# Kernel tuning notes

Hardware: AMD Instinct MI355X
Metric: run time of the kernel (lower is better)

## Reference

```python
import jax, jax.numpy as jnp
import numpy as np

KS = 3      # kernel_size
PAD = 1     # padding
DIL = 2     # dilation


def conv2d(x, w, b=None, stride=1, padding=0):
    out = jax.lax.conv_general_dilated(
        x, w, (stride, stride), [(padding, padding)] * 2,
        dimension_numbers=("NCHW", "OIHW", "NCHW"))
    if b is not None:
        out = out + b[None, :, None, None]
    return out


def setup_inputs() -> dict:
    key = jax.random.key(0)
    ks = jax.random.split(key, 6)
    b, inc, outc, H, W = 2, 256, 256, 96, 96
    x = jax.random.normal(ks[0], (b, inc, H, W), jnp.float32)
    w_p = jax.random.normal(ks[1], (2 * KS * KS, inc, 3, 3), jnp.float32) * 0.01
    b_p = jax.random.normal(ks[2], (2 * KS * KS,), jnp.float32) * 0.01
    w_ad = jax.random.normal(ks[3], (KS, inc, 3, 3), jnp.float32) * 0.01
    b_ad = jax.random.normal(ks[4], (KS,), jnp.float32) * 0.01
    w_conv = jax.random.normal(ks[5], (outc, inc, KS, KS), jnp.float32) * 0.02
    return {"x": x, "w_p": w_p, "b_p": b_p, "w_ad": w_ad, "b_ad": b_ad, "w_conv": w_conv}


def reference(x, w_p, b_p, w_ad, b_ad, w_conv):
    b, c, H, W = x.shape
    N = KS * KS

    offset = conv2d(x, w_p, b_p, stride=1, padding=1)                    # [b,2N,H,W]
    ad_base = 1.0 - jax.nn.sigmoid(conv2d(x, w_ad, b_ad, stride=1, padding=1))  # [b,KS,H,W]
    ad = jnp.tile(ad_base, (1, 2 * KS, 1, 1)) * DIL                      # [b,2N,H,W]

    # p_n: per-kernel-tap offsets (x-part first, then y-part), meshgrid 'ij'
    r = jnp.arange(-(KS - 1) // 2, (KS - 1) // 2 + 1, dtype=jnp.float32)
    pnx, pny = jnp.meshgrid(r, r, indexing="ij")
    p_n = jnp.concatenate([pnx.ravel(), pny.ravel()])[None, :, None, None]  # [1,2N,1,1]

    # p_0: base sampling grid in padded-image coords (starts at 1)
    p0x = jnp.broadcast_to(jnp.arange(1, H + 1, dtype=jnp.float32)[:, None], (H, W))
    p0y = jnp.broadcast_to(jnp.arange(1, W + 1, dtype=jnp.float32)[None, :], (H, W))
    p_0 = jnp.concatenate([jnp.tile(p0x[None, None], (1, N, 1, 1)),
                           jnp.tile(p0y[None, None], (1, N, 1, 1))], axis=1)  # [1,2N,H,W]

    p = p_0 + p_n + offset + ad * p_n                                    # [b,2N,H,W]
    p = jnp.transpose(p, (0, 2, 3, 1))                                   # [b,H,W,2N]

    xp = jnp.pad(x, ((0, 0), (0, 0), (PAD, PAD), (PAD, PAD)))
    Hp, Wp = xp.shape[2], xp.shape[3]

    q_lt = jnp.floor(jax.lax.stop_gradient(p))
    q_rb = q_lt + 1

    def clampxy(q):
        return jnp.concatenate([jnp.clip(q[..., :N], 0, Hp - 1),
                                jnp.clip(q[..., N:], 0, Wp - 1)], -1).astype(jnp.int32)

    q_lt = clampxy(q_lt)
    q_rb = clampxy(q_rb)
    q_lb = jnp.concatenate([q_lt[..., :N], q_rb[..., N:]], -1)
    q_rt = jnp.concatenate([q_rb[..., :N], q_lt[..., N:]], -1)

    mask = jnp.concatenate(
        [(p[..., :N] < PAD) | (p[..., :N] > Hp - 1 - PAD),
         (p[..., N:] < PAD) | (p[..., N:] > Wp - 1 - PAD)], -1)
    mask = jax.lax.stop_gradient(mask).astype(p.dtype)
    floor_p = p - (p - jnp.floor(p))  # == floor(p) but with zero gradient, as in torch
    p = p * (1 - mask) + floor_p * mask
    p = jnp.concatenate([jnp.clip(p[..., :N], 0, Hp - 1),
                         jnp.clip(p[..., N:], 0, Wp - 1)], -1)

    px, py = p[..., :N], p[..., N:]
    f = lambda q: q.astype(p.dtype)
    g_lt = (1 + (f(q_lt[..., :N]) - px)) * (1 + (f(q_lt[..., N:]) - py))
    g_rb = (1 - (f(q_rb[..., :N]) - px)) * (1 - (f(q_rb[..., N:]) - py))
    g_lb = (1 + (f(q_lb[..., :N]) - px)) * (1 - (f(q_lb[..., N:]) - py))
    g_rt = (1 - (f(q_rt[..., :N]) - px)) * (1 + (f(q_rt[..., N:]) - py))

    xf = xp.reshape(b, c, Hp * Wp)

    def gather(xb, q):  # xb [c,L], q [H,W,2N] -> [c,H,W,N]
        idx = q[..., :N] * Wp + q[..., N:]
        return xb[:, idx]

    gq = jax.vmap(gather)
    x_lt = gq(xf, q_lt)
    x_rb = gq(xf, q_rb)
    x_lb = gq(xf, q_lb)
    x_rt = gq(xf, q_rt)

    x_off = (g_lt[:, None] * x_lt + g_rb[:, None] * x_rb +
             g_lb[:, None] * x_lb + g_rt[:, None] * x_rt)  # [b,c,H,W,N]

    # N index k = kx*KS + ky -> place at (i*KS+kx, j*KS+ky)
    x_off = x_off.reshape(b, c, H, W, KS, KS)
    x_off = jnp.transpose(x_off, (0, 1, 2, 4, 3, 5)).reshape(b, c, H * KS, W * KS)

    return conv2d(x_off, w_conv, None, stride=KS, padding=0)  # [b,outc,H,W]
```

## Files before the change

kernel.cpp:

```cpp
#include <hip/hip_runtime.h>
#include <math.h>

typedef unsigned short u16;
typedef unsigned int   u32;

typedef __attribute__((ext_vector_type(8))) _Float16 f16x8;
typedef __attribute__((ext_vector_type(4))) float    f32x4;

#define NB   2
#define C    256
#define H    96
#define W    96
#define HW   (H*W)
#define HP   98
#define OC   256
#define KDIM (9*C)
#define NS   (NB*HW)

#define PARTIAL_OFF  0
#define XP_OFF       13934592
#define AHI_OFF      33603584
#define ALO_OFF      34783232
#define IDX_OFF      35962880
#define G_OFF        38617088

__device__ __forceinline__ u16 h2u(_Float16 h) {
  return __builtin_bit_cast(unsigned short, h);
}
__device__ __forceinline__ void split16(float v, u16& hi, u16& lo) {
  _Float16 h = (_Float16)v;
  float r = v - (float)h;
  _Float16 l = (_Float16)r;
  hi = h2u(h); lo = h2u(l);
}
__device__ __forceinline__ void sync_lds() {
  asm volatile("s_waitcnt lgkmcnt(0)\n\ts_barrier" ::: "memory");
}

__global__ __launch_bounds__(256) void prep1(
    const float* __restrict__ x, const float* __restrict__ w_p,
    const float* __restrict__ w_ad, const float* __restrict__ w_conv,
    float* __restrict__ partial, float* __restrict__ xp,
    u16* __restrict__ A_hi, u16* __restrict__ A_lo) {
  __shared__ float smem[4224];
  int bx = blockIdx.x;
  int tid = threadIdx.x;

  if (bx < 288) {
    int cg = bx & 1; int chunk = (bx >> 1) & 7; int r = bx >> 4;
    int tile = r % 9; int n = r / 9;
    int h0 = (tile / 3) * 32, w0 = (tile % 3) * 32;
    int chB = cg * 11; int chN = cg ? 10 : 11;

    for (int idx = tid; idx < 3168; idx += 256) {
      int tap = idx % 9; int r2 = idx / 9; int chl = r2 % 11; int cc = r2 / 11;
      int ch = chB + chl; int gc = chunk*32 + cc;
      if (ch < 21) {
        float v = (ch < 18) ? w_p[((size_t)ch*C + gc)*9 + tap]
                            : w_ad[((size_t)(ch-18)*C + gc)*9 + tap];
        smem[(cc*11 + chl)*12 + tap] = v;
      }
    }
    __syncthreads();

    int row = tid >> 3, col0 = (tid & 7) * 4;
    int h = h0 + row, w = w0 + col0;

    float acc[11][4];
    #pragma unroll
    for (int i = 0; i < 11; i++)
      { acc[i][0]=0.f; acc[i][1]=0.f; acc[i][2]=0.f; acc[i][3]=0.f; }

    const float* xn = x + (size_t)(n*C + chunk*32) * HW;
    for (int cc = 0; cc < 32; cc++) {
      const float* xc = xn + cc * HW;
      float xr[3][6];
      #pragma unroll
      for (int di = 0; di < 3; di++) {
        int hg = h + di - 1;
        bool hok = ((unsigned)hg < 96u);
        #pragma unroll
        for (int jj = 0; jj < 6; jj++) {
          int wg = w + jj - 1;
          bool ok = hok && ((unsigned)wg < 96u);
          xr[di][jj] = ok ? xc[hg*W + wg] : 0.f;
        }
      }
      #pragma unroll
      for (int chl = 0; chl < 11; chl++) {
        if (chl < chN) {
          const float* wv = &smem[(cc*11 + chl)*12];
          float4 wa = *(const float4*)(wv);
          float4 wb = *(const float4*)(wv + 4);
          float  w8 = wv[8];
          float wt[9] = {wa.x, wa.y, wa.z, wa.w, wb.x, wb.y, wb.z, wb.w, w8};
          #pragma unroll
          for (int di = 0; di < 3; di++)
            #pragma unroll
            for (int dj = 0; dj < 3; dj++) {
              float wgt = wt[di*3 + dj];
              #pragma unroll
              for (int j = 0; j < 4; j++)
                acc[chl][j] = fmaf(xr[di][dj + j], wgt, acc[chl][j]);
            }
        }
      }
    }
    #pragma unroll
    for (int chl = 0; chl < 11; chl++) {
      if (chl < chN) {
        int off = ((chunk*2 + n)*21 + chB + chl)*HW + h*W + w;
        *(float4*)(partial + off) = make_float4(acc[chl][0], acc[chl][1],
                                                acc[chl][2], acc[chl][3]);
      }
    }

  } else if (bx < 1440) {
    int pb = bx - 288;
    int n = pb / 576; int r = pb % 576;
    int cb = r / 144; int hwb = r % 144;
    int c0 = cb * 64, hw0 = hwb * 64;
    int ii = tid & 63; int cl4 = tid >> 6;
    #pragma unroll
    for (int r2 = 0; r2 < 16; r2++) {
      int c_l = cl4*16 + r2;
      smem[c_l*65 + ii] = x[(size_t)(n*C + c0 + c_l)*HW + hw0 + ii];
    }
    __syncthreads();
    int hw = hw0 + ii;
    int h = hw / W, w = hw % W;
    float* dst = xp + ((size_t)(n*HP + h + 1)*HP + (w + 1))*C + c0 + cl4*16;
    #pragma unroll
    for (int q = 0; q < 4; q++) {
      *(float4*)(dst + q*4) = make_float4(smem[(cl4*16 + q*4 + 0)*65 + ii],
                                          smem[(cl4*16 + q*4 + 1)*65 + ii],
                                          smem[(cl4*16 + q*4 + 2)*65 + ii],
                                          smem[(cl4*16 + q*4 + 3)*65 + ii]);
    }

  } else {
    int pb = bx - 1440;
    int t = pb*256 + tid;
    int e0 = t*8;
    int lane = (e0 >> 3) & 63;
    int mi   = (e0 >> 9) & 3;
    int mw   = (e0 >> 11) & 1;
    int rr   = e0 >> 12; int itg = rr % 72; int mo = rr / 72;
    int o = mo*128 + mw*64 + mi*16 + (lane & 15);
    int kcb = itg*32 + (lane >> 4)*8;
    #pragma unroll
    for (int j2 = 0; j2 < 8; j2++) {
      int kc = kcb + j2; int k = kc >> 8; int c = kc & 255;
      float a = w_conv[((size_t)o*C + c)*9 + k];
      u16 hi, lo; split16(a, hi, lo);
      A_hi[e0 + j2] = hi; A_lo[e0 + j2] = lo;
    }
  }
}

__global__ __launch_bounds__(256) void taps2(
    const float* __restrict__ partial, const float* __restrict__ b_p,
    const float* __restrict__ b_ad,
    int* __restrict__ idx_arr, float* __restrict__ g_arr) {
  int e = blockIdx.x * 256 + threadIdx.x;
  int k = e / NS; int s = e % NS;
  int n = s / HW; int hw = s % HW;
  int h = hw / W, w = hw % W;
  int ka = 18 + (k % 3);
  float offx = 0.f, offy = 0.f, za = 0.f;
  #pragma unroll
  for (int chunk = 0; chunk < 8; chunk++) {
    const float* pb2 = partial + (size_t)((chunk*2 + n)*21)*HW + hw;
    offx += pb2[(size_t)k*HW];
    offy += pb2[(size_t)(k+9)*HW];
    za   += pb2[(size_t)ka*HW];
  }
  offx += b_p[k]; offy += b_p[k+9];
  za   += b_ad[k % 3];
  float a2 = 2.0f / (1.0f + expf(za));

  float ri = (float)(k / 3) - 1.0f, rj = (float)(k % 3) - 1.0f;
  float px = (float)(h + 1) + ri + offx + a2 * ri;
  float py = (float)(w + 1) + rj + offy + a2 * rj;
  float fx = floorf(px), fy = floorf(py);
  int qltx = min(max((int)fx, 0), 97);
  int qlty = min(max((int)fy, 0), 97);
  int qrbx = min(max((int)fx + 1, 0), 97);
  int qrby = min(max((int)fy + 1, 0), 97);
  bool mx = (px < 1.0f) || (px > 96.0f);
  bool my = (py < 1.0f) || (py > 96.0f);
  float pxm = mx ? fx : px;
  float pym = my ? fy : py;
  pxm = fminf(fmaxf(pxm, 0.f), 97.f);
  pym = fminf(fmaxf(pym, 0.f), 97.f);
  float glx = 1.0f + ((float)qltx - pxm);
  float grx = 1.0f - ((float)qrbx - pxm);
  float gly = 1.0f + ((float)qlty - pym);
  float gry = 1.0f - ((float)qrby - pym);
  int base = n * HP * HP * C;
  int4 qi;
  qi.x = base + (qltx*HP + qlty)*C;
  qi.y = base + (qrbx*HP + qrby)*C;
  qi.z = base + (qltx*HP + qrby)*C;
  qi.w = base + (qrbx*HP + qlty)*C;
  float4 gg = make_float4(glx*gly, grx*gry, glx*gry, grx*gly);
  *(int4*)(idx_arr + (size_t)e*4) = qi;
  *(float4*)(g_arr  + (size_t)e*4) = gg;
}

__global__ __launch_bounds__(256) void gemm_def(
    const u16* __restrict__ A_hi, const u16* __restrict__ A_lo,
    const float* __restrict__ xp,
    const int* __restrict__ idx_arr, const float* __restrict__ g_arr,
    float* __restrict__ out) {
  __shared__ u16 Bh[2][64*40];
  __shared__ u16 Bl[2][64*40];
  int bx = blockIdx.x;
  int xcd = bx & 7; int jj = bx >> 3;
  int kh = jj & 1; int sbl = jj >> 1;
  int sb = xcd*36 + sbl;
  int s0 = sb * 64;
  int n = s0 / HW; int hw0 = s0 % HW;
  int tid = threadIdx.x;
  int wave = tid >> 6, lane = tid & 63;
  int l16 = lane & 15, quad = lane >> 4;
  int mo = wave >> 1, mw = wave & 1;

  f32x4 acc[4][4];
  f32x4 z4 = {0.f, 0.f, 0.f, 0.f};
  #pragma unroll
  for (int i = 0; i < 4; i++)
    { acc[i][0] = z4; acc[i][1] = z4; acc[i][2] = z4; acc[i][3] = z4; }

  int s_l = tid >> 2; int cs = (tid & 3) * 8;
  int sg = s0 + s_l;

  int4 qi; float4 gg;
  for (int it = 0; it < 36; it++) {
    int itg = kh*36 + it;
    int c0k = (itg & 7) * 32;
    if (it == 0 || (itg & 7) == 0) {
      int k = itg >> 3;
      qi = *(const int4*)(idx_arr + ((size_t)k*NS + sg)*4);
      gg = *(const float4*)(g_arr  + ((size_t)k*NS + sg)*4);
    }
    uint4 aH[4], aL[4];
    int abase = ((mo*72 + itg)*2 + mw)*4;
    #pragma unroll
    for (int mi = 0; mi < 4; mi++) {
      size_t off = ((size_t)(abase + mi) << 9) + lane*8;
      aH[mi] = *(const uint4*)(A_hi + off);
      aL[mi] = *(const uint4*)(A_lo + off);
    }
    const float* p0 = xp + qi.x + c0k + cs;
    const float* p1 = xp + qi.y + c0k + cs;
    const float* p2 = xp + qi.z + c0k + cs;
    const float* p3 = xp + qi.w + c0k + cs;
    float4 t0a = *(const float4*)(p0), t0b = *(const float4*)(p0 + 4);
    float4 t1a = *(const float4*)(p1), t1b = *(const float4*)(p1 + 4);
    float4 t2a = *(const float4*)(p2), t2b = *(const float4*)(p2 + 4);
    float4 t3a = *(const float4*)(p3), t3b = *(const float4*)(p3 + 4);
    float v[8];
    v[0] = gg.x*t0a.x + gg.y*t1a.x + gg.z*t2a.x + gg.w*t3a.x;
    v[1] = gg.x*t0a.y + gg.y*t1a.y + gg.z*t2a.y + gg.w*t3a.y;
    v[2] = gg.x*t0a.z + gg.y*t1a.z + gg.z*t2a.z + gg.w*t3a.z;
    v[3] = gg.x*t0a.w + gg.y*t1a.w + gg.z*t2a.w + gg.w*t3a.w;
    v[4] = gg.x*t0b.x + gg.y*t1b.x + gg.z*t2b.x + gg.w*t3b.x;
    v[5] = gg.x*t0b.y + gg.y*t1b.y + gg.z*t2b.y + gg.w*t3b.y;
    v[6] = gg.x*t0b.z + gg.y*t1b.z + gg.z*t2b.z + gg.w*t3b.z;
    v[7] = gg.x*t0b.w + gg.y*t1b.w + gg.z*t2b.w + gg.w*t3b.w;
    u16 hb[8], lb[8];
    #pragma unroll
    for (int j = 0; j < 8; j++) split16(v[j], hb[j], lb[j]);
    uint4 bph, bpl;
    bph.x = (u32)hb[0] | ((u32)hb[1] << 16); bph.y = (u32)hb[2] | ((u32)hb[3] << 16);
    bph.z = (u32)hb[4] | ((u32)hb[5] << 16); bph.w = (u32)hb[6] | ((u32)hb[7] << 16);
    bpl.x = (u32)lb[0] | ((u32)lb[1] << 16); bpl.y = (u32)lb[2] | ((u32)lb[3] << 16);
    bpl.z = (u32)lb[4] | ((u32)lb[5] << 16); bpl.w = (u32)lb[6] | ((u32)lb[7] << 16);
    int buf = it & 1;
    *(uint4*)(&Bh[buf][s_l*40 + cs]) = bph;
    *(uint4*)(&Bl[buf][s_l*40 + cs]) = bpl;
    sync_lds();
    f16x8 bfh[4], bfl[4];
    #pragma unroll
    for (int ni = 0; ni < 4; ni++) {
      int rr = (ni*16 + l16)*40 + quad*8;
      bfh[ni] = *(const f16x8*)(&Bh[buf][rr]);
      bfl[ni] = *(const f16x8*)(&Bl[buf][rr]);
    }
    #pragma unroll
    for (int mi = 0; mi < 4; mi++) {
      f16x8 fh = __builtin_bit_cast(f16x8, aH[mi]);
      f16x8 fl = __builtin_bit_cast(f16x8, aL[mi]);
      #pragma unroll
      for (int ni = 0; ni < 4; ni++) {
        acc[mi][ni] = __builtin_amdgcn_mfma_f32_16x16x32_f16(fh, bfh[ni], acc[mi][ni], 0, 0, 0);
        acc[mi][ni] = __builtin_amdgcn_mfma_f32_16x16x32_f16(fh, bfl[ni], acc[mi][ni], 0, 0, 0);
        acc[mi][ni] = __builtin_amdgcn_mfma_f32_16x16x32_f16(fl, bfh[ni], acc[mi][ni], 0, 0, 0);
      }
    }
  }
  #pragma unroll
  for (int mi = 0; mi < 4; mi++)
    #pragma unroll
    for (int ni = 0; ni < 4; ni++) {
      int hw = hw0 + ni*16 + l16;
      #pragma unroll
      for (int rr = 0; rr < 4; rr++) {
        int o = wave*64 + mi*16 + quad*4 + rr;
        atomicAdd(&out[(size_t)(n*OC + o)*HW + hw], acc[mi][ni][rr]);
      }
    }
}

extern "C" void kernel_launch(void* const* d_in, const int* in_sizes, int n_in,
                              void* d_out, int out_size, void* d_ws, size_t ws_size,
                              hipStream_t stream) {
  const float* x      = (const float*)d_in[0];
  const float* w_p    = (const float*)d_in[1];
  const float* b_p    = (const float*)d_in[2];
  const float* w_ad   = (const float*)d_in[3];
  const float* b_ad   = (const float*)d_in[4];
  const float* w_conv = (const float*)d_in[5];
  float* out = (float*)d_out;

  char* ws = (char*)d_ws;
  float* partial = (float*)(ws + PARTIAL_OFF);
  float* xp      = (float*)(ws + XP_OFF);
  u16*   A_hi    = (u16*)  (ws + AHI_OFF);
  u16*   A_lo    = (u16*)  (ws + ALO_OFF);
  int*   idx_arr = (int*)  (ws + IDX_OFF);
  float* g_arr   = (float*)(ws + G_OFF);

  hipMemsetAsync(xp, 0, (size_t)NB*HP*HP*C*sizeof(float), stream);
  hipMemsetAsync(out, 0, (size_t)out_size*sizeof(float), stream);

  prep1   <<<1728, 256, 0, stream>>>(x, w_p, w_ad, w_conv, partial, xp, A_hi, A_lo);
  taps2   <<<648,  256, 0, stream>>>(partial, b_p, b_ad, idx_arr, g_arr);
  gemm_def<<<576,  256, 0, stream>>>(A_hi, A_lo, xp, idx_arr, g_arr, out);
}
```

Measured before the change: 248.5 us.

## Compute offset/modulation conv via split-fp16 MFMA GEMM instead of scalar FMA

Replaces the scalar-FMA direct convolution that produced the 21 offset/attention channels with an implicit-GEMM kernel. It runs on MFMA f16 instructions, using a hi/lo split of both operands (three products) to stay close to fp32 accuracy. Weights are pre-split and packed in prep1, and the kernel reads the padded NHWC xp buffer. Each block covers half of K and combines its results with atomicAdd into a zeroed buffer. This removes the per-chunk partial buffer and the 8-way reduction in taps2. The cost is an extra launch, an extra memset, atomics, and the input conv now waits on the xp transpose.

```diff
diff --git a/kernel.cpp b/kernel.cpp
--- a/kernel.cpp
+++ b/kernel.cpp
@@ -17,12 +17,14 @@
 #define KDIM (9*C)
 #define NS   (NB*HW)
 
-#define PARTIAL_OFF  0
-#define XP_OFF       13934592
-#define AHI_OFF      33603584
-#define ALO_OFF      34783232
-#define IDX_OFF      35962880
-#define G_OFF        38617088
+#define XP_OFF    0
+#define AHI_OFF   19668992
+#define ALO_OFF   20848640
+#define A2HI_OFF  22028288
+#define A2LO_OFF  22175744
+#define OFF2_OFF  22323200
+#define IDX_OFF   23871488
+#define G_OFF     26525696
 
 __device__ __forceinline__ u16 h2u(_Float16 h) {
   return __builtin_bit_cast(unsigned short, h);
@@ -40,83 +42,15 @@
 __global__ __launch_bounds__(256) void prep1(
     const float* __restrict__ x, const float* __restrict__ w_p,
     const float* __restrict__ w_ad, const float* __restrict__ w_conv,
-    float* __restrict__ partial, float* __restrict__ xp,
-    u16* __restrict__ A_hi, u16* __restrict__ A_lo) {
-  __shared__ float smem[4224];
+    float* __restrict__ xp,
+    u16* __restrict__ A_hi, u16* __restrict__ A_lo,
+    u16* __restrict__ A2_hi, u16* __restrict__ A2_lo) {
+  __shared__ float smem[64*65];
   int bx = blockIdx.x;
   int tid = threadIdx.x;
 
-  if (bx < 288) {
-    int cg = bx & 1; int chunk = (bx >> 1) & 7; int r = bx >> 4;
-    int tile = r % 9; int n = r / 9;
-    int h0 = (tile / 3) * 32, w0 = (tile % 3) * 32;
-    int chB = cg * 11; int chN = cg ? 10 : 11;
-
-    for (int idx = tid; idx < 3168; idx += 256) {
-      int tap = idx % 9; int r2 = idx / 9; int chl = r2 % 11; int cc = r2 / 11;
-      int ch = chB + chl; int gc = chunk*32 + cc;
-      if (ch < 21) {
-        float v = (ch < 18) ? w_p[((size_t)ch*C + gc)*9 + tap]
-                            : w_ad[((size_t)(ch-18)*C + gc)*9 + tap];
-        smem[(cc*11 + chl)*12 + tap] = v;
-      }
-    }
-    __syncthreads();
-
-    int row = tid >> 3, col0 = (tid & 7) * 4;
-    int h = h0 + row, w = w0 + col0;
-
-    float acc[11][4];
-    #pragma unroll
-    for (int i = 0; i < 11; i++)
-      { acc[i][0]=0.f; acc[i][1]=0.f; acc[i][2]=0.f; acc[i][3]=0.f; }
-
-    const float* xn = x + (size_t)(n*C + chunk*32) * HW;
-    for (int cc = 0; cc < 32; cc++) {
-      const float* xc = xn + cc * HW;
-      float xr[3][6];
-      #pragma unroll
-      for (int di = 0; di < 3; di++) {
-        int hg = h + di - 1;
-        bool hok = ((unsigned)hg < 96u);
-        #pragma unroll
-        for (int jj = 0; jj < 6; jj++) {
-          int wg = w + jj - 1;
-          bool ok = hok && ((unsigned)wg < 96u);
-          xr[di][jj] = ok ? xc[hg*W + wg] : 0.f;
-        }
-      }
-      #pragma unroll
-      for (int chl = 0; chl < 11; chl++) {
-        if (chl < chN) {
-          const float* wv = &smem[(cc*11 + chl)*12];
-          float4 wa = *(const float4*)(wv);
-          float4 wb = *(const float4*)(wv + 4);
-          float  w8 = wv[8];
-          float wt[9] = {wa.x, wa.y, wa.z, wa.w, wb.x, wb.y, wb.z, wb.w, w8};
-          #pragma unroll
-          for (int di = 0; di < 3; di++)
-            #pragma unroll
-            for (int dj = 0; dj < 3; dj++) {
-              float wgt = wt[di*3 + dj];
-              #pragma unroll
-              for (int j = 0; j < 4; j++)
-                acc[chl][j] = fmaf(xr[di][dj + j], wgt, acc[chl][j]);
-            }
-        }
-      }
-    }
-    #pragma unroll
-    for (int chl = 0; chl < 11; chl++) {
-      if (chl < chN) {
-        int off = ((chunk*2 + n)*21 + chB + chl)*HW + h*W + w;
-        *(float4*)(partial + off) = make_float4(acc[chl][0], acc[chl][1],
-                                                acc[chl][2], acc[chl][3]);
-      }
-    }
-
-  } else if (bx < 1440) {
-    int pb = bx - 288;
+  if (bx < 1152) {
+    int pb = bx;
     int n = pb / 576; int r = pb % 576;
     int cb = r / 144; int hwb = r % 144;
     int c0 = cb * 64, hw0 = hwb * 64;
@@ -138,8 +72,8 @@
                                           smem[(cl4*16 + q*4 + 3)*65 + ii]);
     }
 
-  } else {
-    int pb = bx - 1440;
+  } else if (bx < 1440) {
+    int pb = bx - 1152;
     int t = pb*256 + tid;
     int e0 = t*8;
     int lane = (e0 >> 3) & 63;
@@ -155,28 +89,113 @@
       u16 hi, lo; split16(a, hi, lo);
       A_hi[e0 + j2] = hi; A_lo[e0 + j2] = lo;
     }
+
+  } else {
+    int pb = bx - 1440;
+    int t = pb*256 + tid;
+    int e0 = t*8;
+    int lane = (e0 >> 3) & 63;
+    int mi   = (e0 >> 9) & 1;
+    int itg  = e0 >> 10;
+    int o = mi*16 + (lane & 15);
+    int kcb = itg*32 + (lane >> 4)*8;
+    #pragma unroll
+    for (int j2 = 0; j2 < 8; j2++) {
+      int kc = kcb + j2; int tap = kc >> 8; int c = kc & 255;
+      float a = 0.f;
+      if (o < 18)       a = w_p [((size_t)o*C + c)*9 + tap];
+      else if (o < 21)  a = w_ad[((size_t)(o-18)*C + c)*9 + tap];
+      u16 hi, lo; split16(a, hi, lo);
+      A2_hi[e0 + j2] = hi; A2_lo[e0 + j2] = lo;
+    }
   }
 }
 
+__global__ __launch_bounds__(256) void conv_mfma(
+    const u16* __restrict__ A2_hi, const u16* __restrict__ A2_lo,
+    const float* __restrict__ xp, float* __restrict__ off2) {
+  __shared__ u16 Bh[2][64*40];
+  __shared__ u16 Bl[2][64*40];
+  int bx = blockIdx.x;
+  int xcd = bx & 7; int jj = bx >> 3;
+  int kh = jj & 1; int sbl = jj >> 1;
+  int sb = xcd*36 + sbl;
+  int s0 = sb * 64;
+  int tid = threadIdx.x;
+  int wave = tid >> 6, lane = tid & 63;
+  int l16 = lane & 15, quad = lane >> 4;
+
+  f32x4 acc[2];
+  f32x4 z4 = {0.f, 0.f, 0.f, 0.f};
+  acc[0] = z4; acc[1] = z4;
+
+  int s_l = tid >> 2; int cs = (tid & 3) * 8;
+  int sg = s0 + s_l;
+  int n = sg / HW; int hw = sg % HW;
+  int h = hw / W, w = hw % W;
+  const float* sbase = xp + ((size_t)(n*HP + h)*HP + w)*C;
+
+  for (int it = 0; it < 36; it++) {
+    int itg = kh*36 + it;
+    int tap = itg >> 3;
+    int di = tap / 3, dj = tap % 3;
+    int c0k = (itg & 7) * 32;
+    uint4 aH[2], aL[2];
+    #pragma unroll
+    for (int mi = 0; mi < 2; mi++) {
+      size_t off = ((size_t)(itg*2 + mi) << 9) + lane*8;
+      aH[mi] = *(const uint4*)(A2_hi + off);
+      aL[mi] = *(const uint4*)(A2_lo + off);
+    }
+    const float* p0 = sbase + (di*HP + dj)*C + c0k + cs;
+    float4 ta = *(const float4*)(p0), tb = *(const float4*)(p0 + 4);
+    float v[8] = {ta.x, ta.y, ta.z, ta.w, tb.x, tb.y, tb.z, tb.w};
+    u16 hb[8], lb[8];
+    #pragma unroll
+    for (int j = 0; j < 8; j++) split16(v[j], hb[j], lb[j]);
+    uint4 bph, bpl;
+    bph.x = (u32)hb[0] | ((u32)hb[1] << 16); bph.y = (u32)hb[2] | ((u32)hb[3] << 16);
+    bph.z = (u32)hb[4] | ((u32)hb[5] << 16); bph.w = (u32)hb[6] | ((u32)hb[7] << 16);
+    bpl.x = (u32)lb[0] | ((u32)lb[1] << 16); bpl.y = (u32)lb[2] | ((u32)lb[3] << 16);
+    bpl.z = (u32)lb[4] | ((u32)lb[5] << 16); bpl.w = (u32)lb[6] | ((u32)lb[7] << 16);
+    int buf = it & 1;
+    *(uint4*)(&Bh[buf][s_l*40 + cs]) = bph;
+    *(uint4*)(&Bl[buf][s_l*40 + cs]) = bpl;
+    sync_lds();
+    int rr = (wave*16 + l16)*40 + quad*8;
+    f16x8 bfh = *(const f16x8*)(&Bh[buf][rr]);
+    f16x8 bfl = *(const f16x8*)(&Bl[buf][rr]);
+    #pragma unroll
+    for (int mi = 0; mi < 2; mi++) {
+      f16x8 fh = __builtin_bit_cast(f16x8, aH[mi]);
+      f16x8 fl = __builtin_bit_cast(f16x8, aL[mi]);
+      acc[mi] = __builtin_amdgcn_mfma_f32_16x16x32_f16(fh, bfh, acc[mi], 0, 0, 0);
+      acc[mi] = __builtin_amdgcn_mfma_f32_16x16x32_f16(fh, bfl, acc[mi], 0, 0, 0);
+      acc[mi] = __builtin_amdgcn_mfma_f32_16x16x32_f16(fl, bfh, acc[mi], 0, 0, 0);
+    }
+  }
+  int sout = s0 + wave*16 + l16;
+  #pragma unroll
+  for (int mi = 0; mi < 2; mi++)
+    #pragma unroll
+    for (int rr2 = 0; rr2 < 4; rr2++) {
+      int o = mi*16 + quad*4 + rr2;
+      if (o < 21)
+        atomicAdd(&off2[(size_t)o*NS + sout], acc[mi][rr2]);
+    }
+}
+
 __global__ __launch_bounds__(256) void taps2(
-    const float* __restrict__ partial, const float* __restrict__ b_p,
+    const float* __restrict__ off2, const float* __restrict__ b_p,
     const float* __restrict__ b_ad,
     int* __restrict__ idx_arr, float* __restrict__ g_arr) {
   int e = blockIdx.x * 256 + threadIdx.x;
   int k = e / NS; int s = e % NS;
   int n = s / HW; int hw = s % HW;
   int h = hw / W, w = hw % W;
-  int ka = 18 + (k % 3);
-  float offx = 0.f, offy = 0.f, za = 0.f;
-  #pragma unroll
-  for (int chunk = 0; chunk < 8; chunk++) {
-    const float* pb2 = partial + (size_t)((chunk*2 + n)*21)*HW + hw;
-    offx += pb2[(size_t)k*HW];
-    offy += pb2[(size_t)(k+9)*HW];
-    za   += pb2[(size_t)ka*HW];
-  }
-  offx += b_p[k]; offy += b_p[k+9];
-  za   += b_ad[k % 3];
+  float offx = off2[(size_t)k*NS + s]            + b_p[k];
+  float offy = off2[(size_t)(k+9)*NS + s]        + b_p[k+9];
+  float za   = off2[(size_t)(18 + (k%3))*NS + s] + b_ad[k % 3];
   float a2 = 2.0f / (1.0f + expf(za));
 
   float ri = (float)(k / 3) - 1.0f, rj = (float)(k % 3) - 1.0f;
@@ -325,17 +344,21 @@
   float* out = (float*)d_out;
 
   char* ws = (char*)d_ws;
-  float* partial = (float*)(ws + PARTIAL_OFF);
   float* xp      = (float*)(ws + XP_OFF);
   u16*   A_hi    = (u16*)  (ws + AHI_OFF);
   u16*   A_lo    = (u16*)  (ws + ALO_OFF);
+  u16*   A2_hi   = (u16*)  (ws + A2HI_OFF);
+  u16*   A2_lo   = (u16*)  (ws + A2LO_OFF);
+  float* off2    = (float*)(ws + OFF2_OFF);
   int*   idx_arr = (int*)  (ws + IDX_OFF);
   float* g_arr   = (float*)(ws + G_OFF);
 
   hipMemsetAsync(xp, 0, (size_t)NB*HP*HP*C*sizeof(float), stream);
+  hipMemsetAsync(off2, 0, (size_t)21*NS*sizeof(float), stream);
   hipMemsetAsync(out, 0, (size_t)out_size*sizeof(float), stream);
 
-  prep1   <<<1728, 256, 0, stream>>>(x, w_p, w_ad, w_conv, partial, xp, A_hi, A_lo);
-  taps2   <<<648,  256, 0, stream>>>(partial, b_p, b_ad, idx_arr, g_arr);
-  gemm_def<<<576,  256, 0, stream>>>(A_hi, A_lo, xp, idx_arr, g_arr, out);
-}
+  prep1    <<<1476, 256, 0, stream>>>(x, w_p, w_ad, w_conv, xp, A_hi, A_lo, A2_hi, A2_lo);
+  conv_mfma<<<576,  256, 0, stream>>>(A2_hi, A2_lo, xp, off2);
+  taps2    <<<648,  256, 0, stream>>>(off2, b_p, b_ad, idx_arr, g_arr);
+  gemm_def <<<576,  256, 0, stream>>>(A_hi, A_lo, xp, idx_arr, g_arr, out);
+}
```

Result: faster. 219.3 us (-11.8%).
